# Optimization experiments

Hardware: AMD Instinct MI355X
Metric: run time of the kernel (lower is better)

The kernel has to match this reference:

```python
import jax, jax.numpy as jnp
import numpy as np

N = 100000   # nodes
E = 600000   # edges
H = 128      # hidden_dim
G = 1000     # graphs in batch
BN_EPS = 1e-5


def setup_inputs() -> dict:
    key = jax.random.key(0)
    ks = jax.random.split(key, 24)
    inp = {}
    inp['x'] = jax.random.normal(ks[0], (N, 3), dtype=jnp.float32)
    inp['edge_index'] = jax.random.randint(ks[1], (2, E), 0, N, dtype=jnp.int64)
    inp['batch'] = jnp.sort(jax.random.randint(ks[2], (N,), 0, G, dtype=jnp.int64))
    # conv 0 (in=3)
    inp['W1_0'] = jax.random.normal(ks[3], (3, H), dtype=jnp.float32) * 0.3
    inp['b1_0'] = jax.random.normal(ks[4], (H,), dtype=jnp.float32) * 0.02
    inp['g_0'] = jax.random.uniform(ks[5], (H,), dtype=jnp.float32) + 0.5
    inp['be_0'] = jax.random.normal(ks[6], (H,), dtype=jnp.float32) * 0.02
    inp['m_0'] = jax.random.normal(ks[7], (H,), dtype=jnp.float32) * 0.02
    inp['v_0'] = jax.random.uniform(ks[8], (H,), dtype=jnp.float32) + 0.5
    inp['W2_0'] = jax.random.normal(ks[9], (H, H), dtype=jnp.float32) * 0.05
    inp['b2_0'] = jax.random.normal(ks[10], (H,), dtype=jnp.float32) * 0.02
    # convs 1..4 (in=H), stacked on leading axis
    inp['W1s'] = jax.random.normal(ks[11], (4, H, H), dtype=jnp.float32) * 0.05
    inp['b1s'] = jax.random.normal(ks[12], (4, H), dtype=jnp.float32) * 0.02
    inp['gs'] = jax.random.uniform(ks[13], (4, H), dtype=jnp.float32) + 0.5
    inp['bes'] = jax.random.normal(ks[14], (4, H), dtype=jnp.float32) * 0.02
    inp['ms'] = jax.random.normal(ks[15], (4, H), dtype=jnp.float32) * 0.02
    inp['vs'] = jax.random.uniform(ks[16], (4, H), dtype=jnp.float32) + 0.5
    inp['W2s'] = jax.random.normal(ks[17], (4, H, H), dtype=jnp.float32) * 0.05
    inp['b2s'] = jax.random.normal(ks[18], (4, H), dtype=jnp.float32) * 0.02
    inp['Wc'] = jax.random.normal(ks[19], (H, 1), dtype=jnp.float32) * 0.05
    inp['bc'] = jax.random.normal(ks[20], (1,), dtype=jnp.float32) * 0.02
    return inp


def _gin_conv(x, src, dst, W1, b1, g, be, m, v, W2, b2):
    # GINConv with eps=0: mlp(x + sum_{j in N(i)} x_j)
    agg = jax.ops.segment_sum(x[src], dst, num_segments=N)  # [N, d]
    h = x + agg
    h = h @ W1 + b1
    h = g * (h - m) * jax.lax.rsqrt(v + BN_EPS) + be  # BatchNorm (eval)
    h = jax.nn.relu(h)
    h = h @ W2 + b2
    return jax.nn.relu(h)  # outer F.relu in GIN.forward; dropout is identity (eval)


def reference(x, edge_index, batch, W1_0, b1_0, g_0, be_0, m_0, v_0, W2_0, b2_0,
              W1s, b1s, gs, bes, ms, vs, W2s, b2s, Wc, bc):
    src, dst = edge_index[0], edge_index[1]
    h = _gin_conv(x, src, dst, W1_0, b1_0, g_0, be_0, m_0, v_0, W2_0, b2_0)
    for l in range(4):  # fixed small layer loop
        h = _gin_conv(h, src, dst, W1s[l], b1s[l], gs[l], bes[l], ms[l], vs[l], W2s[l], b2s[l])
    pooled = jax.ops.segment_sum(h, batch, num_segments=G)  # [G, H] global_add_pool
    return (pooled @ Wc + bc).reshape(-1)  # [G]
```

## Files before the change

kernel.cpp:

```cpp
#include <hip/hip_runtime.h>

#define NN 100000
#define EE 600000
#define HH 128
#define GG 1000
#define NPAD 100096
#define NBLK2 1564
#define NBLKL 3128

typedef __attribute__((ext_vector_type(8))) short bf16x8;
typedef __attribute__((ext_vector_type(4))) float f32x4;
typedef _Float16 f16;

__device__ inline short f2bf(float x){
    unsigned u = __float_as_uint(x);
    unsigned r = (u + 0x7FFFu + ((u >> 16) & 1u)) >> 16;
    return (short)r;
}
__device__ inline float bf2f(short h){
    unsigned u = ((unsigned)(unsigned short)h) << 16;
    return __uint_as_float(u);
}
__device__ inline float2 cvt2(unsigned u){
    f16 lo = ((const f16*)&u)[0];
    f16 hi = ((const f16*)&u)[1];
    return make_float2((float)lo, (float)hi);
}

__global__ void k_hist(const int* __restrict__ dst, int* __restrict__ cnt){
    int e = blockIdx.x*256 + threadIdx.x;
    if (e < EE) atomicAdd(&cnt[dst[e]], 1);
}

__global__ void k_scan1(const int* __restrict__ cnt, int* __restrict__ excl,
                        int* __restrict__ bsums, int n){
    __shared__ int wsum[4];
    int t = threadIdx.x;
    int idx = blockIdx.x*1024 + t*4;
    int c[4];
#pragma unroll
    for (int i = 0; i < 4; i++) c[i] = (idx+i < n) ? cnt[idx+i] : 0;
    int s = c[0]+c[1]+c[2]+c[3];
    int lane = t & 63, w = t >> 6;
    int x = s;
#pragma unroll
    for (int off = 1; off < 64; off <<= 1){
        int y = __shfl_up(x, off);
        if (lane >= off) x += y;
    }
    if (lane == 63) wsum[w] = x;
    __syncthreads();
    int woff = 0;
    for (int i = 0; i < w; i++) woff += wsum[i];
    int run = woff + x - s;
#pragma unroll
    for (int i = 0; i < 4; i++){
        if (idx+i < n) excl[idx+i] = run;
        run += c[i];
    }
    if (t == 255) bsums[blockIdx.x] = woff + x;
}

__global__ void k_scan2(int* __restrict__ bsums, int nb){
    __shared__ int ws2[2];
    int t = threadIdx.x;
    int v = (t < nb) ? bsums[t] : 0;
    int lane = t & 63, w = t >> 6;
    int x = v;
#pragma unroll
    for (int off = 1; off < 64; off <<= 1){
        int y = __shfl_up(x, off);
        if (lane >= off) x += y;
    }
    if (lane == 63) ws2[w] = x;
    __syncthreads();
    int off0 = (w == 1) ? ws2[0] : 0;
    if (t < nb) bsums[t] = off0 + x - v;
}

__global__ void k_scan3(int* __restrict__ rp, const int* __restrict__ bsums,
                        int* __restrict__ fill, int n){
    int i = blockIdx.x*256 + threadIdx.x;
    if (i < n){
        int r = rp[i] + bsums[i >> 10];
        rp[i] = r;
        fill[i] = r;
    }
    if (i == 0) rp[n] = EE;
}

__global__ void k_place(const int* __restrict__ src, const int* __restrict__ dst,
                        int* __restrict__ fill, int* __restrict__ spk){
    int e = blockIdx.x*256 + threadIdx.x;
    if (e < EE){
        int d = dst[e];
        int p = atomicAdd(&fill[d], 1);
        spk[p] = (src[e] << 4) | (d & 15);
    }
}

__global__ void k_init(const int* __restrict__ batch, int* __restrict__ fill,
                       int* __restrict__ rp_g,
                       const float* __restrict__ W2_0, const float* __restrict__ W1s,
                       const float* __restrict__ W2s, short* __restrict__ Wp){
    int tid = blockIdx.x*256 + threadIdx.x;
    if (tid < NN){
        fill[tid] = 0;
        int b = batch[tid];
        if (tid == 0){
            for (int g = 0; g <= b; g++) rp_g[g] = 0;
        } else {
            int p = batch[tid-1];
            for (int g = p+1; g <= b; g++) rp_g[g] = tid;
        }
        if (tid == NN-1){
            for (int g = b+1; g <= GG; g++) rp_g[g] = NN;
        }
    }
    if (tid < 9*16384){
        int m = tid >> 14;
        int r = tid & 16383;
        int j = r & 7, l = (r >> 3) & 63, ctkc = r >> 9;
        int ct = ctkc & 7, kc = ctkc >> 3;
        int k = kc*32 + ((l >> 4) << 3) + j;
        int n = (ct << 4) + (l & 15);
        const float* W = (m == 0) ? W2_0
                       : (m <= 4) ? (W1s + (size_t)(m-1)*HH*HH)
                                  : (W2s + (size_t)(m-5)*HH*HH);
        float w = W[k*HH + n];
        short hi = f2bf(w);
        short lo = f2bf(w - bf2f(hi));
        short* base = Wp + (size_t)m*32768;
        base[r] = hi;
        base[16384 + r] = lo;
    }
}

__global__ void k_agg3(const float* __restrict__ x, const int* __restrict__ rp,
                       const int* __restrict__ spk, float* __restrict__ y){
    int i = blockIdx.x*256 + threadIdx.x;
    if (i >= NN) return;
    float a0 = x[3*i], a1 = x[3*i+1], a2 = x[3*i+2];
    int b = rp[i], e = rp[i+1];
    for (int k = b; k < e; k++){
        int s = spk[k] >> 4;
        a0 += x[3*s]; a1 += x[3*s+1]; a2 += x[3*s+2];
    }
    y[3*i] = a0; y[3*i+1] = a1; y[3*i+2] = a2;
}


__device__ inline void wave_gemm(const short* __restrict__ sAh,
                                 const short* __restrict__ sAl,
                                 const short* __restrict__ Wp,
                                 int n, int q, f32x4* acc){
    const short* Wh = Wp;
    const short* Wl = Wp + 16384;
    const int l = (q << 4) | n;
#pragma unroll
    for (int ct = 0; ct < 8; ct++) acc[ct] = (f32x4){0.f,0.f,0.f,0.f};
#pragma unroll
    for (int kc = 0; kc < 4; kc++){
        int c = (q << 4) | (n & 8) | ((n & 7) ^ ((q & 1) << 2) ^ kc);
        int pos = kc*512 + c*8;
        bf16x8 ah = *(const bf16x8*)&sAh[pos];
        bf16x8 al = *(const bf16x8*)&sAl[pos];
        const short* ph = Wh + (size_t)(kc*8)*512 + l*8;
        const short* pl = Wl + (size_t)(kc*8)*512 + l*8;
#pragma unroll
        for (int ct = 0; ct < 8; ct++){
            bf16x8 bh = *(const bf16x8*)(ph + ct*512);
            bf16x8 bl = *(const bf16x8*)(pl + ct*512);
            acc[ct] = __builtin_amdgcn_mfma_f32_16x16x32_bf16(ah, bh, acc[ct], 0, 0, 0);
            acc[ct] = __builtin_amdgcn_mfma_f32_16x16x32_bf16(al, bh, acc[ct], 0, 0, 0);
            acc[ct] = __builtin_amdgcn_mfma_f32_16x16x32_bf16(ah, bl, acc[ct], 0, 0, 0);
        }
    }
}

__global__ __launch_bounds__(256, 4)
void k_layer0(const float* __restrict__ y0, const short* __restrict__ Wp,
              const float* __restrict__ W1, const float* __restrict__ b1,
              const float* __restrict__ g, const float* __restrict__ be,
              const float* __restrict__ m, const float* __restrict__ v,
              const float* __restrict__ b2, f16* __restrict__ out){
    __shared__ __align__(16) char smem[32768];
    const int t = threadIdx.x;
    const int w = t >> 6, l = t & 63;
    short* sAh = (short*)(smem + w*8192);
    short* sAl = (short*)(smem + w*8192 + 4096);
    const int R0 = blockIdx.x*64 + w*16;

    {
        int hw = l >> 5, ln = l & 31;
        int c4 = ln << 2;
        int kc1 = ln >> 3, q1 = (ln >> 1) & 3, j1 = (ln & 1) << 2;
        float Wc[3][4], Ac[4], Bc[4];
#pragma unroll
        for (int i = 0; i < 4; i++){
            int c = c4 + i;
            float rs = rsqrtf(v[c] + 1e-5f);
            float sc = g[c]*rs;
            Ac[i] = sc;
            Bc[i] = sc*(b1[c] - m[c]) + be[c];
            Wc[0][i] = W1[c]; Wc[1][i] = W1[HH + c]; Wc[2][i] = W1[2*HH + c];
        }
        float ya[8], yb[8], yc[8];
#pragma unroll
        for (int it = 0; it < 8; it++){
            int node = R0 + hw + (it << 1);
            ya[it] = y0[3*node]; yb[it] = y0[3*node+1]; yc[it] = y0[3*node+2];
        }
#pragma unroll
        for (int it = 0; it < 8; it++){
            int mm = hw + (it << 1);
            float xs[4];
#pragma unroll
            for (int i = 0; i < 4; i++){
                float raw = ya[it]*Wc[0][i] + yb[it]*Wc[1][i] + yc[it]*Wc[2][i];
                xs[i] = fmaxf(fmaf(raw, Ac[i], Bc[i]), 0.f);
            }
            int c = (q1 << 4) | (mm & 8) | ((mm & 7) ^ ((q1 & 1) << 2) ^ kc1);
            int pos = kc1*512 + c*8 + j1;
            unsigned hp[2], lp[2];
#pragma unroll
            for (int i = 0; i < 2; i++){
                unsigned u0 = __float_as_uint(xs[2*i]);
                unsigned u1 = __float_as_uint(xs[2*i+1]);
                float r0 = xs[2*i]   - __uint_as_float(u0 & 0xFFFF0000u);
                float r1 = xs[2*i+1] - __uint_as_float(u1 & 0xFFFF0000u);
                hp[i] = (u0 >> 16) | (u1 & 0xFFFF0000u);
                lp[i] = (__float_as_uint(r0) >> 16) | (__float_as_uint(r1) & 0xFFFF0000u);
            }
            *(uint2*)&sAh[pos] = make_uint2(hp[0], hp[1]);
            *(uint2*)&sAl[pos] = make_uint2(lp[0], lp[1]);
        }
    }
    __asm__ volatile("" ::: "memory");

    const int n = l & 15, q = l >> 4;
    f32x4 acc[8];
    wave_gemm(sAh, sAl, Wp, n, q, acc);
#pragma unroll
    for (int ct = 0; ct < 8; ct++){
        int j = (ct << 4) + n;
        float shv = b2[j];
#pragma unroll
        for (int r = 0; r < 4; r++){
            int row = R0 + q*4 + r;
            out[(size_t)row*HH + j] = (f16)fmaxf(acc[ct][r] + shv, 0.f);
        }
    }
}

__device__ __forceinline__ int sidx(int r, int k){
    return r*128 + (k ^ ((r & 7) << 2));
}

__device__ __forceinline__ void wave_gemm_f32(const float* __restrict__ sF,
                                              const short* __restrict__ Wp,
                                              int l, f32x4* acc){
    const short* Wh = Wp;
    const short* Wl = Wp + 16384;
    const int rw = l & 15, q = l >> 4;
    const int v7 = (rw & 7) << 2;
    const int rbase = rw << 7;
#pragma unroll
    for (int ct = 0; ct < 8; ct++) acc[ct] = (f32x4){0.f,0.f,0.f,0.f};
#pragma unroll
    for (int kc = 0; kc < 4; kc++){
        int k0 = kc*32 + (q << 3);
        float4 fa = *(const float4*)&sF[rbase + ((k0    ) ^ v7)];
        float4 fb = *(const float4*)&sF[rbase + ((k0 + 4) ^ v7)];
        float xs[8] = {fa.x,fa.y,fa.z,fa.w,fb.x,fb.y,fb.z,fb.w};
        bf16x8 ah, al;
#pragma unroll
        for (int i = 0; i < 8; i++){
            unsigned u = __float_as_uint(xs[i]);
            ah[i] = (short)(u >> 16);
            float rv = xs[i] - __uint_as_float(u & 0xFFFF0000u);
            al[i] = (short)(__float_as_uint(rv) >> 16);
        }
        const short* ph = Wh + (size_t)(kc*8)*512 + l*8;
        const short* pl = Wl + (size_t)(kc*8)*512 + l*8;
#pragma unroll
        for (int ct = 0; ct < 8; ct++){
            bf16x8 bh = *(const bf16x8*)(ph + ct*512);
            bf16x8 bl = *(const bf16x8*)(pl + ct*512);
            acc[ct] = __builtin_amdgcn_mfma_f32_16x16x32_bf16(ah, bh, acc[ct], 0, 0, 0);
            acc[ct] = __builtin_amdgcn_mfma_f32_16x16x32_bf16(al, bh, acc[ct], 0, 0, 0);
            acc[ct] = __builtin_amdgcn_mfma_f32_16x16x32_bf16(ah, bl, acc[ct], 0, 0, 0);
        }
    }
}

#define PROC_EDGE(uval, sival) do { \
    int lr_ = (sival) & 15; \
    if (lr_ != cur){ \
        if (cur >= 0){ \
            int off_ = cur*128 + ((2*l) ^ ((cur & 7) << 2)); \
            *(float2*)&sF[off_] = make_float2(acc0, acc1); \
        } \
        cur = lr_; \
        int off_ = lr_*128 + ((2*l) ^ ((lr_ & 7) << 2)); \
        float2 sv_ = *(const float2*)&sF[off_]; \
        acc0 = sv_.x; acc1 = sv_.y; \
    } \
    float2 fv_ = cvt2(uval); \
    acc0 += fv_.x; acc1 += fv_.y; \
} while (0)

#define ISSUE_FULL(U, J) do { \
    _Pragma("unroll") \
    for (int j_ = 0; j_ < 32; j_++){ \
        int sj_ = __builtin_amdgcn_readlane((J), j_) >> 4; \
        U[j_] = A2[(size_t)sj_*64 + l]; \
    } \
} while (0)

#define ISSUE_PART(U, J) do { \
    _Pragma("unroll") \
    for (int j_ = 0; j_ < 32; j_++){ \
        if (j_ < remT){ \
            int sj_ = __builtin_amdgcn_readlane((J), j_) >> 4; \
            U[j_] = A2[(size_t)sj_*64 + l]; \
        } \
    } \
} while (0)

#define PROC_FULL(U, J) do { \
    _Pragma("unroll") \
    for (int j_ = 0; j_ < 32; j_++){ \
        int si_ = __builtin_amdgcn_readlane((J), j_); \
        PROC_EDGE(U[j_], si_); \
    } \
} while (0)

#define PROC_PART(U, J) do { \
    _Pragma("unroll") \
    for (int j_ = 0; j_ < 32; j_++){ \
        if (j_ < remT){ \
            int si_ = __builtin_amdgcn_readlane((J), j_); \
            PROC_EDGE(U[j_], si_); \
        } \
    } \
} while (0)

__global__ __launch_bounds__(128, 4)
void k_layer(const f16* __restrict__ A, const int* __restrict__ rp,
             const int* __restrict__ spk,
             const short* __restrict__ Wp1, const short* __restrict__ Wp2,
             const float* __restrict__ b1, const float* __restrict__ g,
             const float* __restrict__ be, const float* __restrict__ m,
             const float* __restrict__ v, const float* __restrict__ b2,
             f16* __restrict__ out){
    __shared__ __align__(16) float smemf[4096];
    const int t = threadIdx.x;
    const int w = t >> 6, l = t & 63;
    float* sF = smemf + w*2048;
    const int r0w = blockIdx.x*32 + w*16;
    const unsigned* A2 = (const unsigned*)A;

    {
        int half = l >> 5, lm = l & 31;
        int k0 = lm << 2;
#pragma unroll
        for (int i = 0; i < 8; i++){
            int r = (i << 1) + half;
            uint2 u = *(const uint2*)&A2[(size_t)(r0w + r)*64 + (lm << 1)];
            float2 f0 = cvt2(u.x), f1 = cvt2(u.y);
            int base = r*128 + (k0 ^ ((r & 7) << 2));
            *(float4*)&sF[base] = make_float4(f0.x, f0.y, f1.x, f1.y);
        }
    }

    {
        int rlo = r0w < NN ? r0w : NN;
        int rhi = (r0w + 16) < NN ? (r0w + 16) : NN;
        int elo = __builtin_amdgcn_readfirstlane(rp[rlo]);
        int ehi = __builtin_amdgcn_readfirstlane(rp[rhi]);
        int nE  = ehi - elo;
        int nfull = nE >> 5;
        int remT  = nE & 31;
        int lm = l & 31;
        float acc0 = 0.f, acc1 = 0.f;
        int cur = -1;
        unsigned uA[32], uB[32];

        int idxA = spk[elo + lm];
        int idxB = spk[elo + 32 + lm];
        int idxC = spk[elo + 64 + lm];

        if (nfull > 0){
            ISSUE_FULL(uA, idxA);
        } else if (remT > 0){
            ISSUE_PART(uA, idxA);
        }

        int c = 0;
        while (c + 2 <= nfull){
            ISSUE_FULL(uB, idxB);
            int idxD = spk[elo + (c+3)*32 + lm];
            int idxE = spk[elo + (c+4)*32 + lm];
            PROC_FULL(uA, idxA);
            if (c + 2 < nfull){
                ISSUE_FULL(uA, idxC);
            } else if (remT > 0){
                ISSUE_PART(uA, idxC);
            }
            PROC_FULL(uB, idxB);
            idxA = idxC; idxB = idxD; idxC = idxE;
            c += 2;
        }
        if (nfull - c == 1){
            if (remT > 0) ISSUE_PART(uB, idxB);
            PROC_FULL(uA, idxA);
            if (remT > 0) PROC_PART(uB, idxB);
        } else {
            if (remT > 0) PROC_PART(uA, idxA);
        }
        if (cur >= 0){
            int off = cur*128 + ((2*l) ^ ((cur & 7) << 2));
            *(float2*)&sF[off] = make_float2(acc0, acc1);
        }
    }
    __asm__ volatile("" ::: "memory");

    const int n = l & 15, q = l >> 4;

    f32x4 acc[8];
    wave_gemm_f32(sF, Wp1, l, acc);
    __asm__ volatile("" ::: "memory");
#pragma unroll
    for (int ct = 0; ct < 8; ct++){
        int j = (ct << 4) + n;
        float rr = rsqrtf(v[j] + 1e-5f);
        float scv = g[j]*rr;
        float shv = be[j] + scv*(b1[j] - m[j]);
#pragma unroll
        for (int r = 0; r < 4; r++){
            int row = (q << 2) + r;
            float vv = fmaxf(fmaf(acc[ct][r], scv, shv), 0.f);
            sF[sidx(row, j)] = vv;
        }
    }
    __asm__ volatile("" ::: "memory");

    wave_gemm_f32(sF, Wp2, l, acc);
#pragma unroll
    for (int ct = 0; ct < 8; ct++){
        int j = (ct << 4) + n;
        float shv = b2[j];
#pragma unroll
        for (int r = 0; r < 4; r++){
            int row = r0w + (q << 2) + r;
            out[(size_t)row*HH + j] = (f16)fmaxf(acc[ct][r] + shv, 0.f);
        }
    }
}

__global__ void k_pool2(const f16* __restrict__ h, const float* __restrict__ Wc,
                        const float* __restrict__ bc, const int* __restrict__ rp_g,
                        float* __restrict__ out){
    __shared__ float ws[4];
    int g = blockIdx.x, t = threadIdx.x;
    const unsigned* h2 = (const unsigned*)h;
    long beg = (long)rp_g[g]*64, end = (long)rp_g[g+1]*64;
    float s = 0.f;
    for (long i = beg + t; i < end; i += 256){
        unsigned u = h2[i];
        int p = (int)(i & 63);
        float2 fv = cvt2(u);
        s += fv.x*Wc[2*p] + fv.y*Wc[2*p+1];
    }
    int lane = t & 63, w = t >> 6;
#pragma unroll
    for (int off = 32; off > 0; off >>= 1) s += __shfl_down(s, off);
    if (lane == 0) ws[w] = s;
    __syncthreads();
    if (t == 0) out[g] = bc[0] + ws[0] + ws[1] + ws[2] + ws[3];
}

extern "C" void kernel_launch(void* const* d_in, const int* in_sizes, int n_in,
                              void* d_out, int out_size, void* d_ws, size_t ws_size,
                              hipStream_t stream){
    const float* x     = (const float*)d_in[0];
    const int*   ei    = (const int*)d_in[1];
    const int*   batch = (const int*)d_in[2];
    const float* W1_0  = (const float*)d_in[3];
    const float* b1_0  = (const float*)d_in[4];
    const float* g_0   = (const float*)d_in[5];
    const float* be_0  = (const float*)d_in[6];
    const float* m_0   = (const float*)d_in[7];
    const float* v_0   = (const float*)d_in[8];
    const float* W2_0  = (const float*)d_in[9];
    const float* b2_0  = (const float*)d_in[10];
    const float* W1s   = (const float*)d_in[11];
    const float* b1s   = (const float*)d_in[12];
    const float* gs    = (const float*)d_in[13];
    const float* bes   = (const float*)d_in[14];
    const float* ms    = (const float*)d_in[15];
    const float* vs    = (const float*)d_in[16];
    const float* W2s   = (const float*)d_in[17];
    const float* b2s   = (const float*)d_in[18];
    const float* Wc    = (const float*)d_in[19];
    const float* bc    = (const float*)d_in[20];

    f16* H0 = (f16*)d_ws;
    f16* H1 = H0 + (size_t)NPAD*HH;
    int* rp    = (int*)(H1 + (size_t)NPAD*HH);
    int* fill  = rp + (NN + 1);
    int* spk   = fill + NN;
    int* bsums = spk + EE + 128;
    int* rp_g  = bsums + 128;
    size_t off = (size_t)((char*)(rp_g + (GG + 1)) - (char*)d_ws);
    off = (off + 15) & ~(size_t)15;
    short* Wp = (short*)((char*)d_ws + off);
    float* Y  = (float*)H1;

    const int* src = ei;
    const int* dst = ei + EE;

    k_init<<<(9*16384+255)/256, 256, 0, stream>>>(batch, fill, rp_g,
                                                  W2_0, W1s, W2s, Wp);

    k_hist<<<(EE+255)/256, 256, 0, stream>>>(dst, fill);
    k_scan1<<<98, 256, 0, stream>>>(fill, rp, bsums, NN);
    k_scan2<<<1, 128, 0, stream>>>(bsums, 98);
    k_scan3<<<(NN+255)/256, 256, 0, stream>>>(rp, bsums, fill, NN);
    k_place<<<(EE+255)/256, 256, 0, stream>>>(src, dst, fill, spk);

    k_agg3<<<(NN+255)/256, 256, 0, stream>>>(x, rp, spk, Y);
    k_layer0<<<NBLK2, 256, 0, stream>>>(Y, Wp, W1_0, b1_0, g_0, be_0, m_0, v_0,
                                        b2_0, H0);

    f16* cur = H0; f16* oth = H1;
    for (int l = 0; l < 4; l++){
        k_layer<<<NBLKL, 128, 0, stream>>>(cur, rp, spk,
                                           Wp + (size_t)(1+l)*32768,
                                           Wp + (size_t)(5+l)*32768,
                                           b1s + l*HH, gs + l*HH, bes + l*HH,
                                           ms + l*HH, vs + l*HH, b2s + l*HH,
                                           oth);
        f16* tmp = cur; cur = oth; oth = tmp;
    }

    k_pool2<<<GG, 256, 0, stream>>>(cur, Wc, bc, rp_g, (float*)d_out);
}
```

Measured before the change: 433.9 us.

## Process 32 rows per wave in fused GIN layer to reuse weight fragments

```diff
diff --git a/kernel.cpp b/kernel.cpp
--- a/kernel.cpp
+++ b/kernel.cpp
@@ -6,7 +6,7 @@
 #define GG 1000
 #define NPAD 100096
 #define NBLK2 1564
-#define NBLKL 3128
+#define NBLKL 1564
 
 typedef __attribute__((ext_vector_type(8))) short bf16x8;
 typedef __attribute__((ext_vector_type(4))) float f32x4;
@@ -95,7 +95,7 @@
     if (e < EE){
         int d = dst[e];
         int p = atomicAdd(&fill[d], 1);
-        spk[p] = (src[e] << 4) | (d & 15);
+        spk[p] = (src[e] << 5) | (d & 31);
     }
 }
 
@@ -143,7 +143,7 @@
     float a0 = x[3*i], a1 = x[3*i+1], a2 = x[3*i+2];
     int b = rp[i], e = rp[i+1];
     for (int k = b; k < e; k++){
-        int s = spk[k] >> 4;
+        int s = spk[k] >> 5;
         a0 += x[3*s]; a1 += x[3*s+1]; a2 += x[3*s+2];
     }
     y[3*i] = a0; y[3*i+1] = a1; y[3*i+2] = a2;
@@ -257,29 +257,36 @@
     return r*128 + (k ^ ((r & 7) << 2));
 }
 
-__device__ __forceinline__ void wave_gemm_f32(const float* __restrict__ sF,
-                                              const short* __restrict__ Wp,
-                                              int l, f32x4* acc){
+__device__ __forceinline__ void wave_gemm_x2(const float* __restrict__ sF,
+                                             const short* __restrict__ Wp,
+                                             int l, f32x4* acc){
     const short* Wh = Wp;
     const short* Wl = Wp + 16384;
     const int rw = l & 15, q = l >> 4;
     const int v7 = (rw & 7) << 2;
     const int rbase = rw << 7;
 #pragma unroll
-    for (int ct = 0; ct < 8; ct++) acc[ct] = (f32x4){0.f,0.f,0.f,0.f};
+    for (int i = 0; i < 16; i++) acc[i] = (f32x4){0.f,0.f,0.f,0.f};
 #pragma unroll
     for (int kc = 0; kc < 4; kc++){
         int k0 = kc*32 + (q << 3);
-        float4 fa = *(const float4*)&sF[rbase + ((k0    ) ^ v7)];
-        float4 fb = *(const float4*)&sF[rbase + ((k0 + 4) ^ v7)];
-        float xs[8] = {fa.x,fa.y,fa.z,fa.w,fb.x,fb.y,fb.z,fb.w};
-        bf16x8 ah, al;
+        float4 fa0 = *(const float4*)&sF[rbase + ((k0    ) ^ v7)];
+        float4 fb0 = *(const float4*)&sF[rbase + ((k0 + 4) ^ v7)];
+        float4 fa1 = *(const float4*)&sF[2048 + rbase + ((k0    ) ^ v7)];
+        float4 fb1 = *(const float4*)&sF[2048 + rbase + ((k0 + 4) ^ v7)];
+        float x0[8] = {fa0.x,fa0.y,fa0.z,fa0.w,fb0.x,fb0.y,fb0.z,fb0.w};
+        float x1[8] = {fa1.x,fa1.y,fa1.z,fa1.w,fb1.x,fb1.y,fb1.z,fb1.w};
+        bf16x8 ah0, al0, ah1, al1;
 #pragma unroll
         for (int i = 0; i < 8; i++){
-            unsigned u = __float_as_uint(xs[i]);
-            ah[i] = (short)(u >> 16);
-            float rv = xs[i] - __uint_as_float(u & 0xFFFF0000u);
-            al[i] = (short)(__float_as_uint(rv) >> 16);
+            unsigned u0 = __float_as_uint(x0[i]);
+            ah0[i] = (short)(u0 >> 16);
+            float rv0 = x0[i] - __uint_as_float(u0 & 0xFFFF0000u);
+            al0[i] = (short)(__float_as_uint(rv0) >> 16);
+            unsigned u1 = __float_as_uint(x1[i]);
+            ah1[i] = (short)(u1 >> 16);
+            float rv1 = x1[i] - __uint_as_float(u1 & 0xFFFF0000u);
+            al1[i] = (short)(__float_as_uint(rv1) >> 16);
         }
         const short* ph = Wh + (size_t)(kc*8)*512 + l*8;
         const short* pl = Wl + (size_t)(kc*8)*512 + l*8;
@@ -287,22 +294,27 @@
         for (int ct = 0; ct < 8; ct++){
             bf16x8 bh = *(const bf16x8*)(ph + ct*512);
             bf16x8 bl = *(const bf16x8*)(pl + ct*512);
-            acc[ct] = __builtin_amdgcn_mfma_f32_16x16x32_bf16(ah, bh, acc[ct], 0, 0, 0);
-            acc[ct] = __builtin_amdgcn_mfma_f32_16x16x32_bf16(al, bh, acc[ct], 0, 0, 0);
-            acc[ct] = __builtin_amdgcn_mfma_f32_16x16x32_bf16(ah, bl, acc[ct], 0, 0, 0);
+            acc[ct]   = __builtin_amdgcn_mfma_f32_16x16x32_bf16(ah0, bh, acc[ct],   0, 0, 0);
+            acc[ct]   = __builtin_amdgcn_mfma_f32_16x16x32_bf16(al0, bh, acc[ct],   0, 0, 0);
+            acc[ct]   = __builtin_amdgcn_mfma_f32_16x16x32_bf16(ah0, bl, acc[ct],   0, 0, 0);
+            acc[8+ct] = __builtin_amdgcn_mfma_f32_16x16x32_bf16(ah1, bh, acc[8+ct], 0, 0, 0);
+            acc[8+ct] = __builtin_amdgcn_mfma_f32_16x16x32_bf16(al1, bh, acc[8+ct], 0, 0, 0);
+            acc[8+ct] = __builtin_amdgcn_mfma_f32_16x16x32_bf16(ah1, bl, acc[8+ct], 0, 0, 0);
         }
     }
 }
 
 #define PROC_EDGE(uval, sival) do { \
-    int lr_ = (sival) & 15; \
+    int lr_ = (sival) & 31; \
     if (lr_ != cur){ \
         if (cur >= 0){ \
-            int off_ = cur*128 + ((2*l) ^ ((cur & 7) << 2)); \
+            int off_ = ((cur >> 4) << 11) + (cur & 15)*128 \
+                     + ((2*l) ^ ((cur & 7) << 2)); \
             *(float2*)&sF[off_] = make_float2(acc0, acc1); \
         } \
         cur = lr_; \
-        int off_ = lr_*128 + ((2*l) ^ ((lr_ & 7) << 2)); \
+        int off_ = ((lr_ >> 4) << 11) + (lr_ & 15)*128 \
+                 + ((2*l) ^ ((lr_ & 7) << 2)); \
         float2 sv_ = *(const float2*)&sF[off_]; \
         acc0 = sv_.x; acc1 = sv_.y; \
     } \
@@ -313,7 +325,7 @@
 #define ISSUE_FULL(U, J) do { \
     _Pragma("unroll") \
     for (int j_ = 0; j_ < 32; j_++){ \
-        int sj_ = __builtin_amdgcn_readlane((J), j_) >> 4; \
+        int sj_ = __builtin_amdgcn_readlane((J), j_) >> 5; \
         U[j_] = A2[(size_t)sj_*64 + l]; \
     } \
 } while (0)
@@ -322,7 +334,7 @@
     _Pragma("unroll") \
     for (int j_ = 0; j_ < 32; j_++){ \
         if (j_ < remT){ \
-            int sj_ = __builtin_amdgcn_readlane((J), j_) >> 4; \
+            int sj_ = __builtin_amdgcn_readlane((J), j_) >> 5; \
             U[j_] = A2[(size_t)sj_*64 + l]; \
         } \
     } \
@@ -346,7 +358,7 @@
     } \
 } while (0)
 
-__global__ __launch_bounds__(128, 4)
+__global__ __launch_bounds__(128, 2)
 void k_layer(const f16* __restrict__ A, const int* __restrict__ rp,
              const int* __restrict__ spk,
              const short* __restrict__ Wp1, const short* __restrict__ Wp2,
@@ -354,29 +366,30 @@
              const float* __restrict__ be, const float* __restrict__ m,
              const float* __restrict__ v, const float* __restrict__ b2,
              f16* __restrict__ out){
-    __shared__ __align__(16) float smemf[4096];
+    __shared__ __align__(16) float smemf[8192];
     const int t = threadIdx.x;
     const int w = t >> 6, l = t & 63;
-    float* sF = smemf + w*2048;
-    const int r0w = blockIdx.x*32 + w*16;
+    float* sF = smemf + w*4096;
+    const int r0w = blockIdx.x*64 + w*32;
     const unsigned* A2 = (const unsigned*)A;
 
     {
         int half = l >> 5, lm = l & 31;
         int k0 = lm << 2;
 #pragma unroll
-        for (int i = 0; i < 8; i++){
+        for (int i = 0; i < 16; i++){
             int r = (i << 1) + half;
             uint2 u = *(const uint2*)&A2[(size_t)(r0w + r)*64 + (lm << 1)];
             float2 f0 = cvt2(u.x), f1 = cvt2(u.y);
-            int base = r*128 + (k0 ^ ((r & 7) << 2));
+            int rr = r & 15, tt = r >> 4;
+            int base = (tt << 11) + rr*128 + (k0 ^ ((rr & 7) << 2));
             *(float4*)&sF[base] = make_float4(f0.x, f0.y, f1.x, f1.y);
         }
     }
 
     {
         int rlo = r0w < NN ? r0w : NN;
-        int rhi = (r0w + 16) < NN ? (r0w + 16) : NN;
+        int rhi = (r0w + 32) < NN ? (r0w + 32) : NN;
         int elo = __builtin_amdgcn_readfirstlane(rp[rlo]);
         int ehi = __builtin_amdgcn_readfirstlane(rp[rhi]);
         int nE  = ehi - elo;
@@ -420,7 +433,8 @@
             if (remT > 0) PROC_PART(uA, idxA);
         }
         if (cur >= 0){
-            int off = cur*128 + ((2*l) ^ ((cur & 7) << 2));
+            int off = ((cur >> 4) << 11) + (cur & 15)*128
+                    + ((2*l) ^ ((cur & 7) << 2));
             *(float2*)&sF[off] = make_float2(acc0, acc1);
         }
     }
@@ -428,8 +442,8 @@
 
     const int n = l & 15, q = l >> 4;
 
-    f32x4 acc[8];
-    wave_gemm_f32(sF, Wp1, l, acc);
+    f32x4 acc[16];
+    wave_gemm_x2(sF, Wp1, l, acc);
     __asm__ volatile("" ::: "memory");
 #pragma unroll
     for (int ct = 0; ct < 8; ct++){
@@ -438,23 +452,29 @@
         float scv = g[j]*rr;
         float shv = be[j] + scv*(b1[j] - m[j]);
 #pragma unroll
-        for (int r = 0; r < 4; r++){
-            int row = (q << 2) + r;
-            float vv = fmaxf(fmaf(acc[ct][r], scv, shv), 0.f);
-            sF[sidx(row, j)] = vv;
+        for (int tt = 0; tt < 2; tt++){
+#pragma unroll
+            for (int r = 0; r < 4; r++){
+                int row = (q << 2) + r;
+                float vv = fmaxf(fmaf(acc[tt*8 + ct][r], scv, shv), 0.f);
+                sF[(tt << 11) + sidx(row, j)] = vv;
+            }
         }
     }
     __asm__ volatile("" ::: "memory");
 
-    wave_gemm_f32(sF, Wp2, l, acc);
+    wave_gemm_x2(sF, Wp2, l, acc);
 #pragma unroll
     for (int ct = 0; ct < 8; ct++){
         int j = (ct << 4) + n;
         float shv = b2[j];
 #pragma unroll
-        for (int r = 0; r < 4; r++){
-            int row = r0w + (q << 2) + r;
-            out[(size_t)row*HH + j] = (f16)fmaxf(acc[ct][r] + shv, 0.f);
+        for (int tt = 0; tt < 2; tt++){
+#pragma unroll
+            for (int r = 0; r < 4; r++){
+                int row = r0w + (tt << 4) + (q << 2) + r;
+                out[(size_t)row*HH + j] = (f16)fmaxf(acc[tt*8 + ct][r] + shv, 0.f);
+            }
         }
     }
 }
```

Measured after the change: 540.9 us. 1.25x slower.
